# Kernel tuning notes

Measured on AMD Instinct MI355X. Metric: run time of the kernel, lower is better.

## Reference

```python
import jax, jax.numpy as jnp
import numpy as np

B, H, N, C = 4, 16, 1024, 64
D = H * C  # d_model = 1024


def setup_inputs() -> dict:
    key = jax.random.key(0)
    ks = jax.random.split(key, 6)
    q = jax.random.normal(ks[0], (B, H, N, C), dtype=jnp.float32)
    k = jax.random.normal(ks[1], (B, H, N, C), dtype=jnp.float32)
    v = jax.random.normal(ks[2], (B, H, N, C), dtype=jnp.float32)
    pe = jax.random.normal(ks[3], (1, H, N, N), dtype=jnp.float32)
    # Mlp(h*c): fc1 D->D, SiLU, fc2 D->D (stored as [in, out] for x @ W)
    w1 = jax.random.normal(ks[4], (D, D), dtype=jnp.float32) * (D ** -0.5)
    b1 = jnp.zeros((D,), dtype=jnp.float32)
    w2 = jax.random.normal(ks[5], (D, D), dtype=jnp.float32) * (D ** -0.5)
    b2 = jnp.zeros((D,), dtype=jnp.float32)
    return {"q": q, "k": k, "v": v, "pe": pe,
            "w1": w1, "b1": b1, "w2": w2, "b2": b2}


def reference(q, k, v, pe, w1, b1, w2, b2):
    b, h, n, c = q.shape
    scale = c ** (-0.5)
    # scores: [b,h,n,n]; softmax FIRST, then add pe bias (post-softmax bias)
    scores = jnp.einsum('bhnc,bhmc->bhnm', q, k) * scale
    attn = pe + jax.nn.softmax(scores, axis=-1)
    ctx = jnp.einsum('bhnm,bhmc->bhnc', attn, v)
    # [b,h,n,c] -> [b,n,h*c]
    out = ctx.transpose(0, 2, 1, 3).reshape(b, n, h * c)
    # Mlp: fc1 -> SiLU -> fc2 (dropout is identity at eval)
    hdn = jax.nn.silu(out @ w1 + b1)
    return hdn @ w2 + b2
```

## Files before the change

### kernel.cpp

```cpp
#include <hip/hip_runtime.h>

#define B_ 4
#define H_ 16
#define N_ 1024
#define C_ 64
#define D_ 1024

typedef _Float16 half8 __attribute__((ext_vector_type(8)));
typedef _Float16 half4v __attribute__((ext_vector_type(4)));
typedef float f32x4 __attribute__((ext_vector_type(4)));
typedef float f32x16 __attribute__((ext_vector_type(16)));
typedef unsigned int uint4v __attribute__((ext_vector_type(4)));

#define MFMA16(a, b, c) __builtin_amdgcn_mfma_f32_16x16x32_f16(a, b, c, 0, 0, 0)
#define MFMA32(a, b, c) __builtin_amdgcn_mfma_f32_32x32x16_f16(a, b, c, 0, 0, 0)
#define SM_SHIFT 6.0f

static __device__ __forceinline__ unsigned pk2(float a, float b) {
  auto h = __builtin_amdgcn_cvt_pkrtz(a, b);
  return __builtin_bit_cast(unsigned, h);
}
static __device__ __forceinline__ void swap32(unsigned& a, unsigned& b) {
  asm volatile("v_permlane32_swap_b32 %0, %1" : "+v"(a), "+v"(b));
}
static __device__ __forceinline__ void gload16(const void* g, void* l) {
  __builtin_amdgcn_global_load_lds(
      (const __attribute__((address_space(1))) unsigned int*)g,
      (__attribute__((address_space(3))) unsigned int*)l, 16, 0, 0);
}

__global__ __launch_bounds__(256) void transpose_cvt(
    const float* __restrict__ in, _Float16* __restrict__ outp,
    int in_stride, int out_stride, long in_bstride, long out_bstride)
{
  __shared__ float t[64][65];
  const int tid = threadIdx.x;
  const int r0 = blockIdx.x * 64, c0 = blockIdx.y * 64;
  const float* inb = in + (size_t)blockIdx.z * in_bstride;
  _Float16* outb = outp + (size_t)blockIdx.z * out_bstride;
#pragma unroll
  for (int i = 0; i < 4; ++i) {
    int idx = i * 256 + tid;
    int r = idx >> 4, c4 = (idx & 15) << 2;
    float4 a = *(const float4*)(inb + (size_t)(r0 + r) * in_stride + c0 + c4);
    t[r][c4] = a.x; t[r][c4 + 1] = a.y; t[r][c4 + 2] = a.z; t[r][c4 + 3] = a.w;
  }
  __syncthreads();
#pragma unroll
  for (int i = 0; i < 2; ++i) {
    int idx = i * 256 + tid;
    int rr = idx >> 3, c8 = (idx & 7) << 3;
    half8 hv;
#pragma unroll
    for (int j = 0; j < 8; ++j) hv[j] = (_Float16)t[c8 + j][rr];
    *(half8*)(outb + (size_t)(c0 + rr) * out_stride + r0 + c8) = hv;
  }
}

__global__ __launch_bounds__(512, 1) void pev_kernel(
    const float* __restrict__ pe, const _Float16* __restrict__ vth,
    _Float16* __restrict__ xpe)
{
  __shared__ __align__(16) _Float16 a_lds[2][64][72];
  __shared__ __align__(16) _Float16 b_lds[2][256][72];
  const int tid = threadIdx.x;
  const int n0 = blockIdx.x * 64;
  const int h = blockIdx.y;
  const float* peb = pe + (size_t)h * N_ * N_ + (size_t)n0 * N_;

  const int lane = tid & 63, w = tid >> 6;
  const int l15 = lane & 15, quad = lane >> 4;
  const int wrow = (w >> 2) * 32, wcol = (w & 3) * 64;

  const int ar[2] = { tid >> 4, (512 + tid) >> 4 };
  const int ac4 = (tid & 15) << 2;
  const _Float16* bsrc[4];
  int brow[4], bk8[4];
#pragma unroll
  for (int i = 0; i < 4; ++i) {
    int idx = i * 512 + tid;
    int col = idx >> 3, k8 = (idx & 7) << 3;
    int b = col >> 6, c = col & 63;
    bsrc[i] = vth + ((size_t)(b * H_ + h) * C_ + c) * N_ + k8;
    brow[i] = col;
    bk8[i] = k8;
  }

  f32x4 acc[2][4];
#pragma unroll
  for (int rt = 0; rt < 2; ++rt)
#pragma unroll
    for (int ct = 0; ct < 4; ++ct) acc[rt][ct] = (f32x4){0.f, 0.f, 0.f, 0.f};

  float4 areg[2];
  half8 breg[4];
#pragma unroll
  for (int i = 0; i < 2; ++i) areg[i] = *(const float4*)(peb + (size_t)ar[i] * N_ + ac4);
#pragma unroll
  for (int i = 0; i < 4; ++i) breg[i] = *(const half8*)(bsrc[i]);
#pragma unroll
  for (int i = 0; i < 2; ++i) {
    half4v hv = {(_Float16)areg[i].x, (_Float16)areg[i].y,
                 (_Float16)areg[i].z, (_Float16)areg[i].w};
    *(half4v*)&a_lds[0][ar[i]][ac4] = hv;
  }
#pragma unroll
  for (int i = 0; i < 4; ++i) *(half8*)&b_lds[0][brow[i]][bk8[i]] = breg[i];
#pragma unroll
  for (int i = 0; i < 2; ++i)
    areg[i] = *(const float4*)(peb + (size_t)ar[i] * N_ + 64 + ac4);
#pragma unroll
  for (int i = 0; i < 4; ++i) breg[i] = *(const half8*)(bsrc[i] + 64);
  __syncthreads();

  for (int kt = 0; kt < 16; ++kt) {
    const int cur = kt & 1;
    if (kt < 15) {
#pragma unroll
      for (int i = 0; i < 2; ++i) {
        half4v hv = {(_Float16)areg[i].x, (_Float16)areg[i].y,
                     (_Float16)areg[i].z, (_Float16)areg[i].w};
        *(half4v*)&a_lds[cur ^ 1][ar[i]][ac4] = hv;
      }
#pragma unroll
      for (int i = 0; i < 4; ++i) *(half8*)&b_lds[cur ^ 1][brow[i]][bk8[i]] = breg[i];
    }
    if (kt < 14) {
      int m0 = (kt + 2) * 64;
#pragma unroll
      for (int i = 0; i < 2; ++i)
        areg[i] = *(const float4*)(peb + (size_t)ar[i] * N_ + m0 + ac4);
#pragma unroll
      for (int i = 0; i < 4; ++i) breg[i] = *(const half8*)(bsrc[i] + m0);
    }
#pragma unroll
    for (int s = 0; s < 2; ++s) {
      half8 af[2], bf[4];
#pragma unroll
      for (int rt = 0; rt < 2; ++rt)
        af[rt] = *(const half8*)&a_lds[cur][wrow + rt * 16 + l15][s * 32 + quad * 8];
#pragma unroll
      for (int ct = 0; ct < 4; ++ct)
        bf[ct] = *(const half8*)&b_lds[cur][wcol + ct * 16 + l15][s * 32 + quad * 8];
#pragma unroll
      for (int rt = 0; rt < 2; ++rt)
#pragma unroll
        for (int ct = 0; ct < 4; ++ct)
          acc[rt][ct] = MFMA16(af[rt], bf[ct], acc[rt][ct]);
    }
    __syncthreads();
  }

#pragma unroll
  for (int rt = 0; rt < 2; ++rt)
#pragma unroll
    for (int ct = 0; ct < 4; ++ct) {
      int col = wcol + ct * 16 + l15;
      int b = col >> 6, c = col & 63;
#pragma unroll
      for (int r = 0; r < 4; ++r) {
        int nrow = n0 + wrow + rt * 16 + quad * 4 + r;
        xpe[(size_t)(b * N_ + nrow) * D_ + h * C_ + c] = (_Float16)acc[rt][ct][r];
      }
    }
}

__global__ __launch_bounds__(256, 2) void attn_kernel(
    const float* __restrict__ q, const float* __restrict__ k,
    const _Float16* __restrict__ vth, const _Float16* __restrict__ xpe,
    _Float16* __restrict__ Xh)
{
  __shared__ __align__(16) _Float16 ks[2][2][64][72];
  __shared__ float lbuf[128];

  const int tid = threadIdx.x;
  const int bh = blockIdx.x & 63;
  const int qt = blockIdx.x >> 6;
  const int h = bh & (H_ - 1);
  const int b = bh >> 4;
  const int q0 = qt * 128;

  const float* kb = k + (size_t)bh * N_ * C_;
  const _Float16* vb = vth + (size_t)bh * C_ * N_;

  const int lane = tid & 63;
  const int w = tid >> 6;
  const int l31 = lane & 31;
  const int hh = lane >> 5;

  const int sr = tid >> 4, sc4 = (tid & 15) << 2;

  const _Float16* vr0 = vb + (size_t)l31 * N_ + 8 * hh;
  const _Float16* vr1 = vb + (size_t)(32 + l31) * N_ + 8 * hh;

  half8 qf[4];
  const float* qrow = q + ((size_t)bh * N_ + q0 + 32 * w + l31) * C_;
#pragma unroll
  for (int sc = 0; sc < 4; ++sc) {
    const float* qp = qrow + 16 * sc + 8 * hh;
    float4 t0 = *(const float4*)qp;
    float4 t1 = *(const float4*)(qp + 4);
    half8 hv = { (_Float16)(t0.x * 0.125f), (_Float16)(t0.y * 0.125f),
                 (_Float16)(t0.z * 0.125f), (_Float16)(t0.w * 0.125f),
                 (_Float16)(t1.x * 0.125f), (_Float16)(t1.y * 0.125f),
                 (_Float16)(t1.z * 0.125f), (_Float16)(t1.w * 0.125f) };
    qf[sc] = hv;
  }

  f32x16 Os2[2];
  Os2[0] = (f32x16)(0.f); Os2[1] = (f32x16)(0.f);
  float l4[4] = {0.f, 0.f, 0.f, 0.f};

  float4 kreg[8];

#pragma unroll
  for (int s = 0; s < 2; ++s)
#pragma unroll
    for (int i = 0; i < 4; ++i)
      kreg[s * 4 + i] = *(const float4*)(kb + (size_t)(s * 64 + sr + i * 16) * C_ + sc4);
#pragma unroll
  for (int s = 0; s < 2; ++s)
#pragma unroll
    for (int i = 0; i < 4; ++i) {
      float4 kv = kreg[s * 4 + i];
      half4v hk = {(_Float16)kv.x, (_Float16)kv.y, (_Float16)kv.z, (_Float16)kv.w};
      *(half4v*)&ks[0][s][sr + i * 16][sc4] = hk;
    }
#pragma unroll
  for (int s = 0; s < 2; ++s)
#pragma unroll
    for (int i = 0; i < 4; ++i)
      kreg[s * 4 + i] = *(const float4*)(kb + (size_t)(128 + s * 64 + sr + i * 16) * C_ + sc4);
  __syncthreads();

  for (int p = 0; p < 8; ++p) {
    const int cur = p & 1;

    uint4 vfr[2][4][2];
#pragma unroll
    for (int s = 0; s < 2; ++s)
#pragma unroll
      for (int st = 0; st < 4; ++st) {
        const int off = p * 128 + s * 64 + st * 16;
        vfr[s][st][0] = *(const uint4*)(vr0 + off);
        vfr[s][st][1] = *(const uint4*)(vr1 + off);
      }

    if (p < 7) {
#pragma unroll
      for (int s = 0; s < 2; ++s)
#pragma unroll
        for (int i = 0; i < 4; ++i) {
          float4 kv = kreg[s * 4 + i];
          half4v hk = {(_Float16)kv.x, (_Float16)kv.y, (_Float16)kv.z, (_Float16)kv.w};
          *(half4v*)&ks[cur ^ 1][s][sr + i * 16][sc4] = hk;
        }
    }
    if (p < 6) {
      int m0 = (p + 2) * 128;
#pragma unroll
      for (int s = 0; s < 2; ++s)
#pragma unroll
        for (int i = 0; i < 4; ++i)
          kreg[s * 4 + i] = *(const float4*)(kb + (size_t)(m0 + s * 64 + sr + i * 16) * C_ + sc4);
    }

    half8 pa[2][4];
#pragma unroll
    for (int s = 0; s < 2; ++s) {
      f32x16 sacc2[2];
      sacc2[0] = (f32x16)(0.f); sacc2[1] = (f32x16)(0.f);
#pragma unroll
      for (int sc = 0; sc < 4; ++sc) {
        half8 ak0 = *(const half8*)&ks[cur][s][l31][16 * sc + 8 * hh];
        half8 ak1 = *(const half8*)&ks[cur][s][32 + l31][16 * sc + 8 * hh];
        sacc2[0] = MFMA32(ak0, qf[sc], sacc2[0]);
        sacc2[1] = MFMA32(ak1, qf[sc], sacc2[1]);
      }
#pragma unroll
      for (int kbt = 0; kbt < 2; ++kbt) {
        float pv[16];
#pragma unroll
        for (int r = 0; r < 16; ++r) {
          pv[r] = __expf(sacc2[kbt][r] - SM_SHIFT);
          l4[r & 3] += pv[r];
        }
#pragma unroll
        for (int sp = 0; sp < 2; ++sp) {
          const int rb = 8 * sp;
          unsigned wa = pk2(pv[rb + 0], pv[rb + 1]);
          unsigned wb = pk2(pv[rb + 4], pv[rb + 5]);
          unsigned wc = pk2(pv[rb + 2], pv[rb + 3]);
          unsigned wd = pk2(pv[rb + 6], pv[rb + 7]);
          swap32(wa, wb);
          swap32(wc, wd);
          uint4v pw = {wa, wc, wb, wd};
          pa[s][kbt * 2 + sp] = __builtin_bit_cast(half8, pw);
        }
      }
    }

#pragma unroll
    for (int s = 0; s < 2; ++s)
#pragma unroll
      for (int st = 0; st < 4; ++st) {
        Os2[0] = MFMA32(pa[s][st], __builtin_bit_cast(half8, vfr[s][st][0]), Os2[0]);
        Os2[1] = MFMA32(pa[s][st], __builtin_bit_cast(half8, vfr[s][st][1]), Os2[1]);
      }

    __syncthreads();
  }

  float l = (l4[0] + l4[1]) + (l4[2] + l4[3]);
  l += __shfl_xor(l, 32);
  lbuf[32 * w + l31] = 1.0f / l;

#pragma unroll
  for (int reg = 0; reg < 16; ++reg) {
    const int qi = (reg & 3) + 8 * (reg >> 2) + 4 * hh;
    const float li = lbuf[32 * w + qi];
    const size_t row = (size_t)(b * N_ + q0 + 32 * w + qi);
#pragma unroll
    for (int ct = 0; ct < 2; ++ct) {
      size_t o = row * D_ + h * C_ + 32 * ct + l31;
      Xh[o] = (_Float16)(Os2[ct][reg] * li + (float)xpe[o]);
    }
  }
}

template <bool SILU, typename OT>
__global__ __launch_bounds__(256, 2) void mlp_kernel(
    const _Float16* __restrict__ X, const _Float16* __restrict__ Wt,
    const float* __restrict__ bias, OT* __restrict__ Y)
{
  __shared__ __align__(16) _Float16 a_lds[2][128 * 64];
  __shared__ __align__(16) _Float16 b_lds[2][64 * 64];
  const int tid = threadIdx.x;
  const int id = blockIdx.x;
  const int xcd = id & 7, j = id >> 3;
  const int m0 = (xcd * 4 + (j & 3)) * 128;
  const int n0 = (j >> 2) * 64;
  const int lane = tid & 63, w = tid >> 6;
  const int wr = (w >> 1) * 64, wc = (w & 1) * 32;
  const int l15 = lane & 15, quad = lane >> 4;

  const int lrow8 = lane >> 3;
  const int lg = lane & 7;

  f32x4 acc[4][2];
#pragma unroll
  for (int rt = 0; rt < 4; ++rt)
#pragma unroll
    for (int ct = 0; ct < 2; ++ct) acc[rt][ct] = (f32x4){0.f, 0.f, 0.f, 0.f};

#define STAGE_MLP(buf, k0)                                                     \
  {                                                                            \
    int ar0 = w * 32;                                                          \
    int br0 = w * 16;                                                          \
    for (int jj = 0; jj < 4; ++jj) {                                           \
      int r = ar0 + jj * 8 + lrow8;                                            \
      const _Float16* src = X + (size_t)(m0 + r) * D_ + (k0) + ((lg ^ (r & 7)) << 3); \
      gload16(src, &a_lds[buf][(ar0 + jj * 8) * 64]);                          \
    }                                                                          \
    for (int jj = 0; jj < 2; ++jj) {                                           \
      int r = br0 + jj * 8 + lrow8;                                            \
      const _Float16* src = Wt + (size_t)(n0 + r) * D_ + (k0) + ((lg ^ (r & 7)) << 3); \
      gload16(src, &b_lds[buf][(br0 + jj * 8) * 64]);                          \
    }                                                                          \
  }

  STAGE_MLP(0, 0);
  __syncthreads();

  for (int kt = 0; kt < 16; ++kt) {
    const int cur = kt & 1;
    if (kt < 15) STAGE_MLP(cur ^ 1, (kt + 1) * 64);
#pragma unroll
    for (int s = 0; s < 2; ++s) {
      half8 af[4], bf[2];
#pragma unroll
      for (int rt = 0; rt < 4; ++rt) {
        int row = wr + rt * 16 + l15;
        af[rt] = *(const half8*)&a_lds[cur][row * 64 + (((s * 4 + quad) ^ (row & 7)) << 3)];
      }
#pragma unroll
      for (int ct = 0; ct < 2; ++ct) {
        int row = wc + ct * 16 + l15;
        bf[ct] = *(const half8*)&b_lds[cur][row * 64 + (((s * 4 + quad) ^ (row & 7)) << 3)];
      }
#pragma unroll
      for (int rt = 0; rt < 4; ++rt)
#pragma unroll
        for (int ct = 0; ct < 2; ++ct)
          acc[rt][ct] = MFMA16(af[rt], bf[ct], acc[rt][ct]);
    }
    __syncthreads();
  }
#undef STAGE_MLP

  float bv[2];
#pragma unroll
  for (int ct = 0; ct < 2; ++ct) bv[ct] = bias[n0 + wc + ct * 16 + l15];
#pragma unroll
  for (int rt = 0; rt < 4; ++rt)
#pragma unroll
    for (int ct = 0; ct < 2; ++ct)
#pragma unroll
      for (int r = 0; r < 4; ++r) {
        float val = acc[rt][ct][r] + bv[ct];
        if (SILU) val = val / (1.f + __expf(-val));
        int row = m0 + wr + rt * 16 + quad * 4 + r;
        int col = n0 + wc + ct * 16 + l15;
        Y[(size_t)row * D_ + col] = (OT)val;
      }
}

extern "C" void kernel_launch(void* const* d_in, const int* in_sizes, int n_in,
                              void* d_out, int out_size, void* d_ws, size_t ws_size,
                              hipStream_t stream) {
  const float* q  = (const float*)d_in[0];
  const float* k  = (const float*)d_in[1];
  const float* v  = (const float*)d_in[2];
  const float* pe = (const float*)d_in[3];
  const float* w1 = (const float*)d_in[4];
  const float* b1 = (const float*)d_in[5];
  const float* w2 = (const float*)d_in[6];
  const float* b2 = (const float*)d_in[7];
  float* out = (float*)d_out;

  _Float16* Xh  = (_Float16*)d_out;
  _Float16* vth = (_Float16*)((char*)d_out + (size_t)8 * 1024 * 1024);
  _Float16* xpeH1 = (_Float16*)d_ws;
  _Float16* w1t = (_Float16*)((char*)d_ws + (size_t)8 * 1024 * 1024);
  _Float16* w2t = (_Float16*)((char*)d_ws + (size_t)10 * 1024 * 1024);

  transpose_cvt<<<dim3(16, 16, 1), 256, 0, stream>>>(w1, w1t, D_, D_, 0, 0);
  transpose_cvt<<<dim3(16, 16, 1), 256, 0, stream>>>(w2, w2t, D_, D_, 0, 0);
  transpose_cvt<<<dim3(16, 1, B_ * H_), 256, 0, stream>>>(
      v, vth, C_, N_, (long)N_ * C_, (long)N_ * C_);
  pev_kernel<<<dim3(N_ / 64, H_), 512, 0, stream>>>(pe, vth, xpeH1);
  attn_kernel<<<dim3(B_ * H_ * (N_ / 128)), 256, 0, stream>>>(q, k, vth, xpeH1, Xh);
  mlp_kernel<true, _Float16><<<dim3(512), 256, 0, stream>>>(Xh, w1t, b1, xpeH1);
  mlp_kernel<false, float><<<dim3(512), 256, 0, stream>>>(xpeH1, w2t, b2, out);
}
```

Before: 253.9 us.

## Stage V tiles through LDS in attention and triple-buffer MLP loads

The attention kernel now prefetches V tiles into registers and double-buffers them in shared memory alongside K, instead of issuing per-lane global loads right before the PV MFMAs. The aim is to hide V load latency and get coalesced row loads. The MLP GEMM moves from double to triple buffering with a prefetch distance of two and explicit vmcnt waits, dropping the trailing per-iteration __syncthreads. Both changes use more LDS, which could reduce occupancy, and the hand-coded vmcnt count relies on the exact number of loads issued per stage.

```diff
diff --git a/kernel.cpp b/kernel.cpp
--- a/kernel.cpp
+++ b/kernel.cpp
@@ -171,6 +171,7 @@
     _Float16* __restrict__ Xh)
 {
   __shared__ __align__(16) _Float16 ks[2][2][64][72];
+  __shared__ __align__(16) _Float16 vst[2][2][64][72];
   __shared__ float lbuf[128];
 
   const int tid = threadIdx.x;
@@ -189,9 +190,7 @@
   const int hh = lane >> 5;
 
   const int sr = tid >> 4, sc4 = (tid & 15) << 2;
-
-  const _Float16* vr0 = vb + (size_t)l31 * N_ + 8 * hh;
-  const _Float16* vr1 = vb + (size_t)(32 + l31) * N_ + 8 * hh;
+  const int vr = tid >> 3, vc8 = (tid & 7) << 3;
 
   half8 qf[4];
   const float* qrow = q + ((size_t)bh * N_ + q0 + 32 * w + l31) * C_;
@@ -212,14 +211,19 @@
   float l4[4] = {0.f, 0.f, 0.f, 0.f};
 
   float4 kreg[8];
-
-#pragma unroll
-  for (int s = 0; s < 2; ++s)
+  uint4 vreg[4];
+
+#pragma unroll
+  for (int s = 0; s < 2; ++s) {
 #pragma unroll
     for (int i = 0; i < 4; ++i)
       kreg[s * 4 + i] = *(const float4*)(kb + (size_t)(s * 64 + sr + i * 16) * C_ + sc4);
 #pragma unroll
-  for (int s = 0; s < 2; ++s)
+    for (int i = 0; i < 2; ++i)
+      vreg[s * 2 + i] = *(const uint4*)(vb + (size_t)(vr + i * 32) * N_ + s * 64 + vc8);
+  }
+#pragma unroll
+  for (int s = 0; s < 2; ++s) {
 #pragma unroll
     for (int i = 0; i < 4; ++i) {
       float4 kv = kreg[s * 4 + i];
@@ -227,42 +231,46 @@
       *(half4v*)&ks[0][s][sr + i * 16][sc4] = hk;
     }
 #pragma unroll
-  for (int s = 0; s < 2; ++s)
+    for (int i = 0; i < 2; ++i) *(uint4*)&vst[0][s][vr + i * 32][vc8] = vreg[s * 2 + i];
+  }
+#pragma unroll
+  for (int s = 0; s < 2; ++s) {
 #pragma unroll
     for (int i = 0; i < 4; ++i)
       kreg[s * 4 + i] = *(const float4*)(kb + (size_t)(128 + s * 64 + sr + i * 16) * C_ + sc4);
+#pragma unroll
+    for (int i = 0; i < 2; ++i)
+      vreg[s * 2 + i] = *(const uint4*)(vb + (size_t)(vr + i * 32) * N_ + 128 + s * 64 + vc8);
+  }
   __syncthreads();
 
   for (int p = 0; p < 8; ++p) {
     const int cur = p & 1;
-
-    uint4 vfr[2][4][2];
-#pragma unroll
-    for (int s = 0; s < 2; ++s)
-#pragma unroll
-      for (int st = 0; st < 4; ++st) {
-        const int off = p * 128 + s * 64 + st * 16;
-        vfr[s][st][0] = *(const uint4*)(vr0 + off);
-        vfr[s][st][1] = *(const uint4*)(vr1 + off);
-      }
-
     if (p < 7) {
 #pragma unroll
-      for (int s = 0; s < 2; ++s)
+      for (int s = 0; s < 2; ++s) {
 #pragma unroll
         for (int i = 0; i < 4; ++i) {
           float4 kv = kreg[s * 4 + i];
           half4v hk = {(_Float16)kv.x, (_Float16)kv.y, (_Float16)kv.z, (_Float16)kv.w};
           *(half4v*)&ks[cur ^ 1][s][sr + i * 16][sc4] = hk;
         }
+#pragma unroll
+        for (int i = 0; i < 2; ++i)
+          *(uint4*)&vst[cur ^ 1][s][vr + i * 32][vc8] = vreg[s * 2 + i];
+      }
     }
     if (p < 6) {
       int m0 = (p + 2) * 128;
 #pragma unroll
-      for (int s = 0; s < 2; ++s)
+      for (int s = 0; s < 2; ++s) {
 #pragma unroll
         for (int i = 0; i < 4; ++i)
           kreg[s * 4 + i] = *(const float4*)(kb + (size_t)(m0 + s * 64 + sr + i * 16) * C_ + sc4);
+#pragma unroll
+        for (int i = 0; i < 2; ++i)
+          vreg[s * 2 + i] = *(const uint4*)(vb + (size_t)(vr + i * 32) * N_ + m0 + s * 64 + vc8);
+      }
     }
 
     half8 pa[2][4];
@@ -304,8 +312,10 @@
     for (int s = 0; s < 2; ++s)
 #pragma unroll
       for (int st = 0; st < 4; ++st) {
-        Os2[0] = MFMA32(pa[s][st], __builtin_bit_cast(half8, vfr[s][st][0]), Os2[0]);
-        Os2[1] = MFMA32(pa[s][st], __builtin_bit_cast(half8, vfr[s][st][1]), Os2[1]);
+        half8 bv0 = *(const half8*)&vst[cur][s][l31][16 * st + 8 * hh];
+        half8 bv1 = *(const half8*)&vst[cur][s][32 + l31][16 * st + 8 * hh];
+        Os2[0] = MFMA32(pa[s][st], bv0, Os2[0]);
+        Os2[1] = MFMA32(pa[s][st], bv1, Os2[1]);
       }
 
     __syncthreads();
@@ -333,8 +343,8 @@
     const _Float16* __restrict__ X, const _Float16* __restrict__ Wt,
     const float* __restrict__ bias, OT* __restrict__ Y)
 {
-  __shared__ __align__(16) _Float16 a_lds[2][128 * 64];
-  __shared__ __align__(16) _Float16 b_lds[2][64 * 64];
+  __shared__ __align__(16) _Float16 a_lds[3][128 * 64];
+  __shared__ __align__(16) _Float16 b_lds[3][64 * 64];
   const int tid = threadIdx.x;
   const int id = blockIdx.x;
   const int xcd = id & 7, j = id >> 3;
@@ -370,11 +380,18 @@
   }
 
   STAGE_MLP(0, 0);
-  __syncthreads();
+  STAGE_MLP(1, 64);
 
   for (int kt = 0; kt < 16; ++kt) {
-    const int cur = kt & 1;
-    if (kt < 15) STAGE_MLP(cur ^ 1, (kt + 1) * 64);
+    const int cur = kt % 3;
+    if (kt < 15) asm volatile("s_waitcnt vmcnt(6)" ::: "memory");
+    else         asm volatile("s_waitcnt vmcnt(0)" ::: "memory");
+    __builtin_amdgcn_sched_barrier(0);
+    __builtin_amdgcn_s_barrier();
+    if (kt < 14) {
+      const int nb = (kt + 2) % 3;
+      STAGE_MLP(nb, (kt + 2) * 64);
+    }
 #pragma unroll
     for (int s = 0; s < 2; ++s) {
       half8 af[4], bf[2];
@@ -394,7 +411,6 @@
         for (int ct = 0; ct < 2; ++ct)
           acc[rt][ct] = MFMA16(af[rt], bf[ct], acc[rt][ct]);
     }
-    __syncthreads();
   }
 #undef STAGE_MLP
 
```

Measured after the change: 244.1 us. -3.9%, faster.
